# Performance work log

Hardware: AMD Instinct MI355X
Metric: run time of the kernel (lower is better)

## Reference

```python
import jax, jax.numpy as jnp
import numpy as np

ALPHA = 0.2   # LeakyReLU negative slope
EPS = 1e-8
N_NODES = 100000
N_EDGES = 1600000
D_IN = 128
D_OUT = 128


def setup_inputs() -> dict:
    key = jax.random.key(0)
    k1, k2, k3, k4, k5 = jax.random.split(key, 5)
    h = jax.random.normal(k1, (N_NODES, D_IN), dtype=jnp.float32)
    edge_index = jax.random.randint(k2, (2, N_EDGES), 0, N_NODES, dtype=jnp.int32)
    edge_weight = jax.random.uniform(k3, (N_EDGES,), dtype=jnp.float32)
    # xavier-ish scaled params
    W = jax.random.normal(k4, (D_OUT, D_IN), dtype=jnp.float32) * (1.0 / np.sqrt(D_IN))
    a = jax.random.normal(k5, (1, 2 * D_OUT), dtype=jnp.float32) * (1.0 / np.sqrt(2 * D_OUT))
    return {"h": h, "edge_index": edge_index, "edge_weight": edge_weight, "W": W, "a": a}


def reference(h, edge_index, edge_weight, W, a):
    num_nodes = h.shape[0]
    Wh = h @ W.T                                   # [N, D_OUT]
    src, dst = edge_index[0], edge_index[1]
    d_out = Wh.shape[1]
    a_src = a[0, :d_out]                           # a^T [Wh_i || Wh_j] split into two dots
    a_dst = a[0, d_out:]
    Wh_src = Wh[src]                               # [E, D_OUT] edge gather
    e = Wh_src @ a_src + Wh[dst] @ a_dst           # [E]
    e = jnp.where(e >= 0, e, ALPHA * e)            # LeakyReLU
    e = e * edge_weight
    # segment softmax over edges sharing dst; torch init-to-zero amax => max(seg_max, 0)
    seg_max = jax.ops.segment_max(e, dst, num_segments=num_nodes)
    seg_max = jnp.maximum(seg_max, 0.0)
    ex = jnp.exp(e - seg_max[dst])
    seg_sum = jax.ops.segment_sum(ex, dst, num_segments=num_nodes)
    att = ex / (seg_sum[dst] + EPS)                # [E]
    # weighted scatter-add aggregation (dropout is identity in eval/p=0)
    h_prime = jax.ops.segment_sum(att[:, None] * Wh_src, dst, num_segments=num_nodes)
    return h_prime
```

## Files before the change

kernel.cpp:

```cpp
#include <hip/hip_runtime.h>
#include <hip/hip_bf16.h>
#include <math.h>

#define D_FEAT 128
#define ALPHA 0.2f
#define EPS 1e-8f

#define BSHIFT 7
#define BNODES 128
#define NB_MAX 800
#define NB_PAD 1024
#define CAP_B 2432
#define CCHUNK 2048

typedef __bf16 bf16x8 __attribute__((ext_vector_type(8)));
typedef _Float16 f16x8 __attribute__((ext_vector_type(8)));
typedef _Float16 f16x2 __attribute__((ext_vector_type(2)));
typedef float f32x4 __attribute__((ext_vector_type(4)));

__device__ __forceinline__ void split_bf16(const float* __restrict__ p,
                                           bf16x8& hi, bf16x8& lo)
{
    f32x4 a = *(const f32x4*)p;
    f32x4 b = *(const f32x4*)(p + 4);
#pragma unroll
    for (int j = 0; j < 4; ++j) {
        float x = a[j]; __bf16 xh = (__bf16)x;
        hi[j] = xh; lo[j] = (__bf16)(x - (float)xh);
        float y = b[j]; __bf16 yh = (__bf16)y;
        hi[j + 4] = yh; lo[j + 4] = (__bf16)(y - (float)yh);
    }
}

__global__ __launch_bounds__(256) void presplit_w(
    const float* __restrict__ W, __bf16* __restrict__ Whi, __bf16* __restrict__ Wlo)
{
    const int i = blockIdx.x * 256 + threadIdx.x;
    const float x = W[i];
    const __bf16 xh = (__bf16)x;
    Whi[i] = xh;
    Wlo[i] = (__bf16)(x - (float)xh);
}

__global__ __launch_bounds__(256) void gemm_s_kernel(
    const float* __restrict__ h,
    const __bf16* __restrict__ Whi, const __bf16* __restrict__ Wlo,
    _Float16* __restrict__ Whf, int N)
{
    const int wave = threadIdx.x >> 6;
    const int lane = threadIdx.x & 63;
    const int row0 = blockIdx.x * 128 + wave * 32;
    if (row0 >= N) return;

    const int l15 = lane & 15;
    const int quad = lane >> 4;

    bf16x8 ahi[2][4], alo[2][4];
#pragma unroll
    for (int m = 0; m < 2; ++m) {
        int arow = row0 + m * 16 + l15;
        if (arow >= N) arow = N - 1;
#pragma unroll
        for (int kk = 0; kk < 4; ++kk)
            split_bf16(h + (size_t)arow * D_FEAT + kk * 32 + quad * 8,
                       ahi[m][kk], alo[m][kk]);
    }

    f32x4 acc[2][8];
#pragma unroll
    for (int m = 0; m < 2; ++m)
#pragma unroll
        for (int n = 0; n < 8; ++n) acc[m][n] = (f32x4){0.f, 0.f, 0.f, 0.f};

#pragma unroll
    for (int kk = 0; kk < 4; ++kk) {
#pragma unroll
        for (int n = 0; n < 8; ++n) {
            const size_t boff = (size_t)(n * 16 + l15) * D_FEAT + kk * 32 + quad * 8;
            const bf16x8 bhi = *(const bf16x8*)(Whi + boff);
            const bf16x8 blo = *(const bf16x8*)(Wlo + boff);
#pragma unroll
            for (int m = 0; m < 2; ++m) {
                acc[m][n] = __builtin_amdgcn_mfma_f32_16x16x32_bf16(ahi[m][kk], bhi, acc[m][n], 0, 0, 0);
                acc[m][n] = __builtin_amdgcn_mfma_f32_16x16x32_bf16(ahi[m][kk], blo, acc[m][n], 0, 0, 0);
                acc[m][n] = __builtin_amdgcn_mfma_f32_16x16x32_bf16(alo[m][kk], bhi, acc[m][n], 0, 0, 0);
            }
        }
    }

#pragma unroll
    for (int m = 0; m < 2; ++m) {
        const int rbase = row0 + m * 16;
#pragma unroll
        for (int n = 0; n < 8; ++n) {
            const int col = n * 16 + l15;
#pragma unroll
            for (int r = 0; r < 4; ++r) {
                const int row = rbase + quad * 4 + r;
                if (row < N) Whf[(size_t)row * D_FEAT + col] = (_Float16)acc[m][n][r];
            }
        }
    }
}

__global__ __launch_bounds__(256) void bin_sort_local(
    const int* __restrict__ src, const int* __restrict__ dst,
    const float* __restrict__ ew,
    int* __restrict__ gcur, uint2* __restrict__ bin, int E, int NB)
{
    __shared__ uint2 srt[CCHUNK];
    __shared__ unsigned short sbkt[CCHUNK];
    __shared__ int lhist[NB_PAD];
    __shared__ int loff[NB_PAD];
    __shared__ int lcur[NB_PAD];
    __shared__ int gbase[NB_PAD];
    __shared__ int sh[256];

    const int t = threadIdx.x;
    const int i0 = blockIdx.x * CCHUNK + t * 8;

    lhist[t] = 0; lhist[t + 256] = 0; lhist[t + 512] = 0; lhist[t + 768] = 0;
    __syncthreads();

    int n = E - i0; n = n < 0 ? 0 : (n > 8 ? 8 : n);
    int ss[8], dd[8];
    float wwv[8];
    unsigned meta[8];
    int bb[8];

    if (n == 8) {
        const int4 sa = *(const int4*)(src + i0);
        const int4 sb = *(const int4*)(src + i0 + 4);
        const int4 da = *(const int4*)(dst + i0);
        const int4 db = *(const int4*)(dst + i0 + 4);
        const float4 wa = *(const float4*)(ew + i0);
        const float4 wb = *(const float4*)(ew + i0 + 4);
        ss[0] = sa.x; ss[1] = sa.y; ss[2] = sa.z; ss[3] = sa.w;
        ss[4] = sb.x; ss[5] = sb.y; ss[6] = sb.z; ss[7] = sb.w;
        dd[0] = da.x; dd[1] = da.y; dd[2] = da.z; dd[3] = da.w;
        dd[4] = db.x; dd[5] = db.y; dd[6] = db.z; dd[7] = db.w;
        wwv[0] = wa.x; wwv[1] = wa.y; wwv[2] = wa.z; wwv[3] = wa.w;
        wwv[4] = wb.x; wwv[5] = wb.y; wwv[6] = wb.z; wwv[7] = wb.w;
    } else {
        for (int k = 0; k < n; ++k) {
            ss[k] = src[i0 + k]; dd[k] = dst[i0 + k]; wwv[k] = ew[i0 + k];
        }
    }
#pragma unroll
    for (int k = 0; k < 8; ++k) {
        if (k < n) {
            const int d = dd[k];
            bb[k] = d >> BSHIFT;
            meta[k] = (unsigned)ss[k] | ((unsigned)(d & (BNODES - 1)) << 17);
            atomicAdd(&lhist[bb[k]], 1);
        }
    }
    __syncthreads();

    const int v0 = lhist[4 * t];
    const int v1 = lhist[4 * t + 1];
    const int v2 = lhist[4 * t + 2];
    const int v3 = lhist[4 * t + 3];
    const int ts = v0 + v1 + v2 + v3;
    sh[t] = ts;
    __syncthreads();
    for (int off = 1; off < 256; off <<= 1) {
        int x = (t >= off) ? sh[t - off] : 0;
        __syncthreads();
        sh[t] += x;
        __syncthreads();
    }
    int run = sh[t] - ts;
    loff[4 * t] = run;     lcur[4 * t] = run;     run += v0;
    loff[4 * t + 1] = run; lcur[4 * t + 1] = run; run += v1;
    loff[4 * t + 2] = run; lcur[4 * t + 2] = run; run += v2;
    loff[4 * t + 3] = run; lcur[4 * t + 3] = run;
    const int total = sh[255];

    for (int b = t; b < NB; b += 256) {
        const int c = lhist[b];
        gbase[b] = c ? atomicAdd(&gcur[b], c) : 0;
    }
    __syncthreads();

#pragma unroll
    for (int k = 0; k < 8; ++k) {
        if (k < n) {
            const int p = atomicAdd(&lcur[bb[k]], 1);
            srt[p] = make_uint2(meta[k], __float_as_uint(wwv[k]));
            sbkt[p] = (unsigned short)bb[k];
        }
    }
    __syncthreads();

    for (int i = t; i < total; i += 256) {
        const int b = sbkt[i];
        const int gpos = gbase[b] + (i - loff[b]);
        if (gpos < CAP_B)
            bin[(size_t)b * CAP_B + gpos] = srt[i];
    }
}

__global__ __launch_bounds__(512) void sort_aggregate(
    const int* __restrict__ gcur, const uint2* __restrict__ bin,
    const _Float16* __restrict__ Whf, const float* __restrict__ a,
    float* __restrict__ out, int N)
{
    __shared__ uint2 srec[CAP_B];
    __shared__ int lhist[BNODES];
    __shared__ int loff[BNODES];
    __shared__ int lcur[BNODES];
    __shared__ int sh[BNODES];

    const int t = threadIdx.x;
    const int b = blockIdx.x;
    const size_t base = (size_t)b * CAP_B;
    const int node0 = b << BSHIFT;
    const int nnodes = min(BNODES, N - node0);
    int cnt = gcur[b];
    if (cnt > CAP_B) cnt = CAP_B;

    if (t < BNODES) lhist[t] = 0;
    __syncthreads();

    for (int i = t; i < cnt; i += 512)
        atomicAdd(&lhist[(bin[base + i].x >> 17) & (BNODES - 1)], 1);
    __syncthreads();

    int hv = 0;
    if (t < BNODES) { hv = lhist[t]; sh[t] = hv; }
    __syncthreads();
    for (int off = 1; off < BNODES; off <<= 1) {
        int x = (t >= off && t < BNODES) ? sh[t - off] : 0;
        __syncthreads();
        if (t < BNODES) sh[t] += x;
        __syncthreads();
    }
    if (t < BNODES) { loff[t] = sh[t] - hv; lcur[t] = sh[t] - hv; }
    __syncthreads();

    for (int i = t; i < cnt; i += 512) {
        const uint2 r = bin[base + i];
        const unsigned dl = (r.x >> 17) & (BNODES - 1);
        const int p = atomicAdd(&lcur[dl], 1);
        srec[p] = make_uint2(r.x & 0x1FFFFu, r.y);
    }
    __syncthreads();

    const int wave = t >> 6;
    const int lane = t & 63;
    const int quad = lane >> 4;
    const int c0 = (lane & 15) * 8;

    float asv[8];
#pragma unroll
    for (int i = 0; i < 8; ++i) asv[i] = a[c0 + i];
    const float ad0 = a[D_FEAT + 2 * lane];
    const float ad1 = a[D_FEAT + 2 * lane + 1];

    for (int nd = wave; nd < nnodes; nd += 8) {
        const int rb = loff[nd];
        const int cnt_n = lhist[nd];
        const int node = node0 + nd;

        const f16x2 dv = *(const f16x2*)(Whf + (size_t)node * D_FEAT + 2 * lane);
        float sd = (float)dv[0] * ad0 + (float)dv[1] * ad1;
#pragma unroll
        for (int off = 1; off < 64; off <<= 1)
            sd += __shfl_xor(sd, off, 64);

        float acc[8];
#pragma unroll
        for (int i = 0; i < 8; ++i) acc[i] = 0.f;
        float ssum = 0.f;

        int j = 0;
        for (; j + 15 < cnt_n; j += 16) {
            uint2 m[4];
#pragma unroll
            for (int g = 0; g < 4; ++g) m[g] = srec[rb + j + g * 4 + quad];
            f16x8 v[4];
#pragma unroll
            for (int g = 0; g < 4; ++g)
                v[g] = *(const f16x8*)(Whf + (size_t)m[g].x * D_FEAT + c0);
#pragma unroll
            for (int g = 0; g < 4; ++g) {
                float vf[8];
#pragma unroll
                for (int i = 0; i < 8; ++i) vf[i] = (float)v[g][i];
                float dp = vf[0] * asv[0];
#pragma unroll
                for (int i = 1; i < 8; ++i) dp += vf[i] * asv[i];
                dp += __shfl_xor(dp, 1, 64);
                dp += __shfl_xor(dp, 2, 64);
                dp += __shfl_xor(dp, 4, 64);
                dp += __shfl_xor(dp, 8, 64);
                float e = dp + sd;
                e = (e >= 0.f) ? e : ALPHA * e;
                e *= __uint_as_float(m[g].y);
                const float ex = __expf(e);
                ssum += ex;
#pragma unroll
                for (int i = 0; i < 8; ++i) acc[i] += ex * vf[i];
            }
        }
        for (; j < cnt_n; j += 4) {
            const int je = j + quad;
            const int jc = je < cnt_n ? je : cnt_n - 1;
            const uint2 m = srec[rb + jc];
            const f16x8 v = *(const f16x8*)(Whf + (size_t)m.x * D_FEAT + c0);
            float vf[8];
#pragma unroll
            for (int i = 0; i < 8; ++i) vf[i] = (float)v[i];
            float dp = vf[0] * asv[0];
#pragma unroll
            for (int i = 1; i < 8; ++i) dp += vf[i] * asv[i];
            dp += __shfl_xor(dp, 1, 64);
            dp += __shfl_xor(dp, 2, 64);
            dp += __shfl_xor(dp, 4, 64);
            dp += __shfl_xor(dp, 8, 64);
            float e = dp + sd;
            e = (e >= 0.f) ? e : ALPHA * e;
            e *= __uint_as_float(m.y);
            float ex = __expf(e);
            if (je >= cnt_n) ex = 0.f;
            ssum += ex;
#pragma unroll
            for (int i = 0; i < 8; ++i) acc[i] += ex * vf[i];
        }
        ssum += __shfl_xor(ssum, 16, 64);
        ssum += __shfl_xor(ssum, 32, 64);
        const float inv = 1.f / (ssum + EPS);
#pragma unroll
        for (int i = 0; i < 8; ++i) {
            acc[i] += __shfl_xor(acc[i], 16, 64);
            acc[i] += __shfl_xor(acc[i], 32, 64);
            acc[i] *= inv;
        }
        if (lane < 16) {
            f32x4 r0, r1;
            r0[0] = acc[0]; r0[1] = acc[1]; r0[2] = acc[2]; r0[3] = acc[3];
            r1[0] = acc[4]; r1[1] = acc[5]; r1[2] = acc[6]; r1[3] = acc[7];
            float* po = out + (size_t)node * D_FEAT + c0;
            *(f32x4*)po = r0;
            *(f32x4*)(po + 4) = r1;
        }
    }
}

extern "C" void kernel_launch(void* const* d_in, const int* in_sizes, int n_in,
                              void* d_out, int out_size, void* d_ws, size_t ws_size,
                              hipStream_t stream) {
    const float* h  = (const float*)d_in[0];
    const int* eidx = (const int*)d_in[1];
    const float* ew = (const float*)d_in[2];
    const float* W  = (const float*)d_in[3];
    const float* a  = (const float*)d_in[4];
    float* out      = (float*)d_out;

    const int N = in_sizes[0] / D_FEAT;
    const int E = in_sizes[2];
    const int* src = eidx;
    const int* dst = eidx + E;

    const int NB = (N + BNODES - 1) / BNODES;

    char* ws = (char*)d_ws;
    size_t off = 0;
    int*      gcur = (int*)(ws + off);      off += (size_t)NB_MAX * 4;
    off = (off + 15) & ~(size_t)15;
    __bf16*   Whi  = (__bf16*)(ws + off);   off += (size_t)D_FEAT * D_FEAT * 2;
    __bf16*   Wlo  = (__bf16*)(ws + off);   off += (size_t)D_FEAT * D_FEAT * 2;
    uint2*    bin  = (uint2*)(ws + off);    off += (size_t)NB_MAX * CAP_B * 8;
    _Float16* Whf  = (_Float16*)(ws + off); off += (size_t)N * D_FEAT * 2;

    hipMemsetAsync(gcur, 0, (size_t)NB * 4, stream);

    presplit_w<<<64, 256, 0, stream>>>(W, Whi, Wlo);
    gemm_s_kernel<<<(N + 127) / 128, 256, 0, stream>>>(h, Whi, Wlo, Whf, N);
    bin_sort_local<<<(E + CCHUNK - 1) / CCHUNK, 256, 0, stream>>>(
        src, dst, ew, gcur, bin, E, NB);
    sort_aggregate<<<NB, 512, 0, stream>>>(gcur, bin, Whf, a, out, N);
}
```

Measured before the change: 290.3 us.

## Precompute per-node attention dot products and exp weights before aggregation

Adds a small kernel that computes each node's source and destination attention scores once, and stores them in workspace. The aggregation kernel now computes each edge's exp weight during the local counting-sort scatter, and sums the weights per node from shared memory. The per-edge gather loop is left doing only a weighted accumulate, with no per-edge dot product, shuffles or exp. In exchange it adds one kernel launch and a scattered read of s_src per edge. The sum is done in a separate pass over shared memory.

```diff
diff --git a/kernel.cpp b/kernel.cpp
--- a/kernel.cpp
+++ b/kernel.cpp
@@ -100,6 +100,34 @@
                 if (row < N) Whf[(size_t)row * D_FEAT + col] = (_Float16)acc[m][n][r];
             }
         }
+    }
+}
+
+__global__ __launch_bounds__(256) void a_dots(
+    const _Float16* __restrict__ Whf, const float* __restrict__ a,
+    float* __restrict__ s_src, float* __restrict__ s_dst, int N)
+{
+    const int wave = threadIdx.x >> 6;
+    const int lane = threadIdx.x & 63;
+    const float as0 = a[2 * lane];
+    const float as1 = a[2 * lane + 1];
+    const float ad0 = a[D_FEAT + 2 * lane];
+    const float ad1 = a[D_FEAT + 2 * lane + 1];
+    const int r0 = blockIdx.x * 32 + wave * 8;
+#pragma unroll
+    for (int k = 0; k < 8; ++k) {
+        const int row = r0 + k;
+        if (row >= N) return;
+        const f16x2 v = *(const f16x2*)(Whf + (size_t)row * D_FEAT + 2 * lane);
+        const float v0 = (float)v[0], v1 = (float)v[1];
+        float ps = v0 * as0 + v1 * as1;
+        float pd = v0 * ad0 + v1 * ad1;
+#pragma unroll
+        for (int off = 1; off < 64; off <<= 1) {
+            ps += __shfl_xor(ps, off, 64);
+            pd += __shfl_xor(pd, off, 64);
+        }
+        if (lane == 0) { s_src[row] = ps; s_dst[row] = pd; }
     }
 }
 
@@ -203,10 +231,12 @@
 
 __global__ __launch_bounds__(512) void sort_aggregate(
     const int* __restrict__ gcur, const uint2* __restrict__ bin,
-    const _Float16* __restrict__ Whf, const float* __restrict__ a,
+    const _Float16* __restrict__ Whf,
+    const float* __restrict__ s_src, const float* __restrict__ s_dst,
     float* __restrict__ out, int N)
 {
     __shared__ uint2 srec[CAP_B];
+    __shared__ float sdl[BNODES];
     __shared__ int lhist[BNODES];
     __shared__ int loff[BNODES];
     __shared__ int lcur[BNODES];
@@ -220,7 +250,10 @@
     int cnt = gcur[b];
     if (cnt > CAP_B) cnt = CAP_B;
 
-    if (t < BNODES) lhist[t] = 0;
+    if (t < BNODES) {
+        lhist[t] = 0;
+        sdl[t] = (node0 + t < N) ? s_dst[node0 + t] : 0.f;
+    }
     __syncthreads();
 
     for (int i = t; i < cnt; i += 512)
@@ -241,9 +274,14 @@
 
     for (int i = t; i < cnt; i += 512) {
         const uint2 r = bin[base + i];
+        const unsigned s = r.x & 0x1FFFFu;
         const unsigned dl = (r.x >> 17) & (BNODES - 1);
+        float e = s_src[s] + sdl[dl];
+        e = (e >= 0.f) ? e : ALPHA * e;
+        e *= __uint_as_float(r.y);
+        const float ex = __expf(e);
         const int p = atomicAdd(&lcur[dl], 1);
-        srec[p] = make_uint2(r.x & 0x1FFFFu, r.y);
+        srec[p] = make_uint2(s, __float_as_uint(ex));
     }
     __syncthreads();
 
@@ -252,27 +290,21 @@
     const int quad = lane >> 4;
     const int c0 = (lane & 15) * 8;
 
-    float asv[8];
-#pragma unroll
-    for (int i = 0; i < 8; ++i) asv[i] = a[c0 + i];
-    const float ad0 = a[D_FEAT + 2 * lane];
-    const float ad1 = a[D_FEAT + 2 * lane + 1];
-
     for (int nd = wave; nd < nnodes; nd += 8) {
         const int rb = loff[nd];
         const int cnt_n = lhist[nd];
-        const int node = node0 + nd;
-
-        const f16x2 dv = *(const f16x2*)(Whf + (size_t)node * D_FEAT + 2 * lane);
-        float sd = (float)dv[0] * ad0 + (float)dv[1] * ad1;
+
+        float ssum = 0.f;
+        for (int jj = lane; jj < cnt_n; jj += 64)
+            ssum += __uint_as_float(srec[rb + jj].y);
 #pragma unroll
         for (int off = 1; off < 64; off <<= 1)
-            sd += __shfl_xor(sd, off, 64);
+            ssum += __shfl_xor(ssum, off, 64);
+        const float inv = 1.f / (ssum + EPS);
 
         float acc[8];
 #pragma unroll
         for (int i = 0; i < 8; ++i) acc[i] = 0.f;
-        float ssum = 0.f;
 
         int j = 0;
         for (; j + 15 < cnt_n; j += 16) {
@@ -285,52 +317,31 @@
                 v[g] = *(const f16x8*)(Whf + (size_t)m[g].x * D_FEAT + c0);
 #pragma unroll
             for (int g = 0; g < 4; ++g) {
-                float vf[8];
-#pragma unroll
-                for (int i = 0; i < 8; ++i) vf[i] = (float)v[g][i];
-                float dp = vf[0] * asv[0];
-#pragma unroll
-                for (int i = 1; i < 8; ++i) dp += vf[i] * asv[i];
-                dp += __shfl_xor(dp, 1, 64);
-                dp += __shfl_xor(dp, 2, 64);
-                dp += __shfl_xor(dp, 4, 64);
-                dp += __shfl_xor(dp, 8, 64);
-                float e = dp + sd;
-                e = (e >= 0.f) ? e : ALPHA * e;
-                e *= __uint_as_float(m[g].y);
-                const float ex = __expf(e);
-                ssum += ex;
-#pragma unroll
-                for (int i = 0; i < 8; ++i) acc[i] += ex * vf[i];
+                const float a0 = __uint_as_float(m[g].y);
+#pragma unroll
+                for (int i = 0; i < 8; ++i) acc[i] += a0 * (float)v[g][i];
             }
+        }
+        for (; j + 7 < cnt_n; j += 8) {
+            const uint2 m0 = srec[rb + j + quad];
+            const uint2 m1 = srec[rb + j + 4 + quad];
+            const float a0 = __uint_as_float(m0.y);
+            const float a1 = __uint_as_float(m1.y);
+            const f16x8 v0 = *(const f16x8*)(Whf + (size_t)m0.x * D_FEAT + c0);
+            const f16x8 v1 = *(const f16x8*)(Whf + (size_t)m1.x * D_FEAT + c0);
+#pragma unroll
+            for (int i = 0; i < 8; ++i)
+                acc[i] += a0 * (float)v0[i] + a1 * (float)v1[i];
         }
         for (; j < cnt_n; j += 4) {
             const int je = j + quad;
             const int jc = je < cnt_n ? je : cnt_n - 1;
             const uint2 m = srec[rb + jc];
+            const float a0 = (je < cnt_n) ? __uint_as_float(m.y) : 0.f;
             const f16x8 v = *(const f16x8*)(Whf + (size_t)m.x * D_FEAT + c0);
-            float vf[8];
-#pragma unroll
-            for (int i = 0; i < 8; ++i) vf[i] = (float)v[i];
-            float dp = vf[0] * asv[0];
-#pragma unroll
-            for (int i = 1; i < 8; ++i) dp += vf[i] * asv[i];
-            dp += __shfl_xor(dp, 1, 64);
-            dp += __shfl_xor(dp, 2, 64);
-            dp += __shfl_xor(dp, 4, 64);
-            dp += __shfl_xor(dp, 8, 64);
-            float e = dp + sd;
-            e = (e >= 0.f) ? e : ALPHA * e;
-            e *= __uint_as_float(m.y);
-            float ex = __expf(e);
-            if (je >= cnt_n) ex = 0.f;
-            ssum += ex;
-#pragma unroll
-            for (int i = 0; i < 8; ++i) acc[i] += ex * vf[i];
-        }
-        ssum += __shfl_xor(ssum, 16, 64);
-        ssum += __shfl_xor(ssum, 32, 64);
-        const float inv = 1.f / (ssum + EPS);
+#pragma unroll
+            for (int i = 0; i < 8; ++i) acc[i] += a0 * (float)v[i];
+        }
 #pragma unroll
         for (int i = 0; i < 8; ++i) {
             acc[i] += __shfl_xor(acc[i], 16, 64);
@@ -341,7 +352,7 @@
             f32x4 r0, r1;
             r0[0] = acc[0]; r0[1] = acc[1]; r0[2] = acc[2]; r0[3] = acc[3];
             r1[0] = acc[4]; r1[1] = acc[5]; r1[2] = acc[6]; r1[3] = acc[7];
-            float* po = out + (size_t)node * D_FEAT + c0;
+            float* po = out + (size_t)(node0 + nd) * D_FEAT + c0;
             *(f32x4*)po = r0;
             *(f32x4*)(po + 4) = r1;
         }
@@ -367,7 +378,9 @@
 
     char* ws = (char*)d_ws;
     size_t off = 0;
-    int*      gcur = (int*)(ws + off);      off += (size_t)NB_MAX * 4;
+    int*      gcur  = (int*)(ws + off);     off += (size_t)NB_MAX * 4;
+    float*    s_src = (float*)(ws + off);   off += (size_t)N * 4;
+    float*    s_dst = (float*)(ws + off);   off += (size_t)N * 4;
     off = (off + 15) & ~(size_t)15;
     __bf16*   Whi  = (__bf16*)(ws + off);   off += (size_t)D_FEAT * D_FEAT * 2;
     __bf16*   Wlo  = (__bf16*)(ws + off);   off += (size_t)D_FEAT * D_FEAT * 2;
@@ -378,7 +391,8 @@
 
     presplit_w<<<64, 256, 0, stream>>>(W, Whi, Wlo);
     gemm_s_kernel<<<(N + 127) / 128, 256, 0, stream>>>(h, Whi, Wlo, Whf, N);
+    a_dots<<<(N + 31) / 32, 256, 0, stream>>>(Whf, a, s_src, s_dst, N);
     bin_sort_local<<<(E + CCHUNK - 1) / CCHUNK, 256, 0, stream>>>(
         src, dst, ew, gcur, bin, E, NB);
-    sort_aggregate<<<NB, 512, 0, stream>>>(gcur, bin, Whf, a, out, N);
-}
+    sort_aggregate<<<NB, 512, 0, stream>>>(gcur, bin, Whf, s_src, s_dst, out, N);
+}
```

After: 288.9 us. Within noise of the previous version (-0.5%).
